# Performance work log

Hardware: AMD Instinct MI355X
Metric: run time of the kernel (lower is better)

## Reference

```python
import jax, jax.numpy as jnp
import numpy as np

B, T, D, H, L = 16, 4096, 256, 256, 2


def setup_inputs() -> dict:
    key = jax.random.key(0)
    ks = jax.random.split(key, 9)
    s = 1.0 / np.sqrt(H)
    u = lambda k, shape: jax.random.uniform(k, shape, jnp.float32, -s, s)
    return {
        "x": jax.random.normal(ks[0], (B, T, D), jnp.float32),
        "W_ih": u(ks[1], (4 * H, D)),
        "W_hh": u(ks[2], (4 * H, H)),
        "b_ih": u(ks[3], (4 * H,)),
        "b_hh": u(ks[4], (4 * H,)),
        "W_lin": u(ks[5], (L, H)),
        "b_lin": u(ks[6], (L,)),
        "fw_att": jnp.full((1, H), 0.001, jnp.float32),
        "bw_att": jnp.full((1, H), 0.001, jnp.float32),
    }


def _lstm(x, W_ih, W_hh, b_ih, b_hh):
    # x: [B, T, D] -> lstm_out: [B, T, H], torch gate order (i, f, g, o)
    x_proj = jnp.einsum("btd,gd->btg", x, W_ih) + b_ih + b_hh  # [B, T, 4H]
    h0 = jnp.zeros((x.shape[0], W_hh.shape[1]), x.dtype)
    c0 = jnp.zeros_like(h0)

    def step(carry, xp):
        h, c = carry
        gates = xp + h @ W_hh.T
        i, f, g, o = jnp.split(gates, 4, axis=-1)
        c = jax.nn.sigmoid(f) * c + jax.nn.sigmoid(i) * jnp.tanh(g)
        h = jax.nn.sigmoid(o) * jnp.tanh(c)
        return (h, c), h

    _, hs = jax.lax.scan(step, (h0, c0), jnp.swapaxes(x_proj, 0, 1))
    return jnp.swapaxes(hs, 0, 1)


def reference(x, W_ih, W_hh, b_ih, b_hh, W_lin, b_lin, fw_att, bw_att):
    lstm_out = _lstm(x, W_ih, W_hh, b_ih, b_hh)  # [B, T, H]
    logits = jnp.einsum("bth,lh->btl", lstm_out, W_lin) + b_lin
    # argmax gate is integer-valued in torch -> no grad path
    g = jax.lax.stop_gradient(jnp.argmax(logits, axis=-1).astype(lstm_out.dtype))[..., None]
    w = g * lstm_out  # [B, T, H]
    inc = jnp.cumsum(w, axis=1)
    prefix = inc - w                         # sum over j < i (exclusive)
    suffix = inc[:, -1:, :] - inc            # sum over j > i (exclusive)
    return 2.0 * lstm_out + prefix * fw_att + suffix * bw_att
```

## Files before the change

kernel.cpp:

```cpp
#include <hip/hip_runtime.h>
#include <cstdint>
#include <cstddef>

#define T_SEQ 4096
#define BATCH 16
#define HID   256
#define GATES 1024
#define DIN   256

typedef _Float16 h2 __attribute__((ext_vector_type(2)));
typedef _Float16 h8 __attribute__((ext_vector_type(8)));
typedef float    f4 __attribute__((ext_vector_type(4)));

#define NREG 100
#define LDSW_DW 28
#define LDSW_BYTES (GATES * LDSW_DW * 4)
#define HBUF_BYTES (2 * HID * 2)
#define GBUF_BYTES (2 * 2 * HID * 4)
#define K2_LDS (LDSW_BYTES + HBUF_BYTES + GBUF_BYTES + 32)

__device__ __forceinline__ float dot2f(h2 a, h2 b, float c) {
#if __has_builtin(__builtin_amdgcn_fdot2)
  return __builtin_amdgcn_fdot2(a, b, c, false);
#else
  return c + (float)a[0] * (float)b[0] + (float)a[1] * (float)b[1];
#endif
}

__device__ __forceinline__ float sigmf_(float x) {
  x = fminf(fmaxf(x, -30.0f), 30.0f);
  return 1.0f / (1.0f + __expf(-x));
}
__device__ __forceinline__ float tanhf_(float x) {
  x = fminf(fmaxf(x, -15.0f), 15.0f);
  const float e = __expf(2.0f * x);
  return (e - 1.0f) / (e + 1.0f);
}

__global__ __launch_bounds__(256) void k1_xproj(
    const float* __restrict__ x, const float* __restrict__ Wih,
    const float* __restrict__ bih, const float* __restrict__ bhh,
    _Float16* __restrict__ xp) {
  const int bid = blockIdx.x;
  const int mt = bid >> 4;
  const int nt = bid & 15;
  const int tid = threadIdx.x;
  const int wv = tid >> 6;
  const int l  = tid & 63;
  const int lr = l & 15;
  const int lq = l >> 4;

  const int arow = mt * 64 + wv * 16 + lr;
  const float* xr = x + (size_t)arow * DIN;

  f4 acc[4] = {};
  #pragma unroll
  for (int ks = 0; ks < 8; ++ks) {
    const int k0 = ks * 32 + lq * 8;
    const float4 a1 = *(const float4*)(xr + k0);
    const float4 a2 = *(const float4*)(xr + k0 + 4);
    const h8 af = { (_Float16)a1.x, (_Float16)a1.y, (_Float16)a1.z, (_Float16)a1.w,
                    (_Float16)a2.x, (_Float16)a2.y, (_Float16)a2.z, (_Float16)a2.w };
    #pragma unroll
    for (int n = 0; n < 4; ++n) {
      const int col = nt * 64 + n * 16 + lr;
      const float* wr = Wih + (size_t)col * DIN + k0;
      const float4 b1 = *(const float4*)wr;
      const float4 b2 = *(const float4*)(wr + 4);
      const h8 bf = { (_Float16)b1.x, (_Float16)b1.y, (_Float16)b1.z, (_Float16)b1.w,
                      (_Float16)b2.x, (_Float16)b2.y, (_Float16)b2.z, (_Float16)b2.w };
      acc[n] = __builtin_amdgcn_mfma_f32_16x16x32_f16(af, bf, acc[n], 0, 0, 0);
    }
  }
  #pragma unroll
  for (int n = 0; n < 4; ++n) {
    const int col = nt * 64 + n * 16 + lr;
    const float bias = bih[col] + bhh[col];
    #pragma unroll
    for (int r = 0; r < 4; ++r) {
      const int row = mt * 64 + wv * 16 + lq * 4 + r;
      xp[(size_t)row * GATES + col] = (_Float16)(acc[n][r] + bias);
    }
  }
}

__global__ __launch_bounds__(512, 2) void k2_lstm(
    const _Float16* __restrict__ xp, const float* __restrict__ Whh,
    const float* __restrict__ Wlin, const float* __restrict__ blin,
    const float* __restrict__ fw, const float* __restrict__ bw,
    float* __restrict__ out, float* __restrict__ tot) {
  extern __shared__ __align__(16) char smem[];
  h2*       ldsW  = (h2*)smem;
  _Float16* hbufP = (_Float16*)(smem + LDSW_BYTES);
  float*    gbufP = (float*)(smem + LDSW_BYTES + HBUF_BYTES);
  float*    pbufP = (float*)(smem + LDSW_BYTES + HBUF_BYTES + GBUF_BYTES);

  const int b   = blockIdx.x;
  const int tid = threadIdx.x;
  const int r0  = tid;
  const int r1  = tid + 512;
  const bool lower = (tid < 256);
  const int j = tid & 255;

  if (tid < 256) { hbufP[tid] = (_Float16)0.0f; hbufP[256 + tid] = (_Float16)0.0f; }

  h2 wA[NREG], wB[NREG];
  {
    const float2* w0p = (const float2*)(Whh + (size_t)r0 * HID);
    const float2* w1p = (const float2*)(Whh + (size_t)r1 * HID);
    #pragma unroll
    for (int i = 0; i < NREG; ++i) {
      const float2 f0 = w0p[i]; const float2 f1 = w1p[i];
      wA[i] = (h2){ (_Float16)f0.x, (_Float16)f0.y };
      wB[i] = (h2){ (_Float16)f1.x, (_Float16)f1.y };
    }
  }
  {
    const float2* wr0 = (const float2*)(Whh + (size_t)r0 * HID + 2 * NREG);
    const float2* wr1 = (const float2*)(Whh + (size_t)r1 * HID + 2 * NREG);
    #pragma unroll
    for (int i = 0; i < LDSW_DW; ++i) {
      const float2 f0 = wr0[i]; const float2 f1 = wr1[i];
      ldsW[(size_t)r0 * LDSW_DW + i] = (h2){ (_Float16)f0.x, (_Float16)f0.y };
      ldsW[(size_t)r1 * LDSW_DW + i] = (h2){ (_Float16)f1.x, (_Float16)f1.y };
    }
  }

  float fwj = 0.f, dfw = 0.f, dwj = 0.f, db = 0.f;
  if (lower) {
    fwj = fw[j];
    const float bwj = bw[j];
    dfw = fwj - bwj;
    dwj = Wlin[HID + j] - Wlin[j];
    db  = blin[1] - blin[0];
  }

  float creg = 0.0f, incj = 0.0f;

  const _Float16* xpb = xp + (size_t)b * T_SEQ * GATES;
  float* outb = out + (size_t)b * T_SEQ * HID;

  _Float16 x0a = xpb[r0],          x0b = xpb[r1];
  _Float16 x1a = xpb[GATES + r0],  x1b = xpb[GATES + r1];

  __syncthreads();

  for (int t = 0; t < T_SEQ; ++t) {
    const int pt = t & 1;
    const int pr = pt ^ 1;

    int tp = t + 2; if (tp > T_SEQ - 1) tp = T_SEQ - 1;
    const _Float16 x2a = xpb[(size_t)tp * GATES + r0];
    const _Float16 x2b = xpb[(size_t)tp * GATES + r1];

    float a0 = (float)x0a;
    float a1 = (float)x0b;

    const h8* hb8 = (const h8*)(hbufP + pr * HID);
    #pragma unroll
    for (int c = 0; c < 25; ++c) {
      const h8 hv = hb8[c];
      const h2 hp0 = { hv[0], hv[1] }, hp1 = { hv[2], hv[3] },
               hp2 = { hv[4], hv[5] }, hp3 = { hv[6], hv[7] };
      a0 = dot2f(wA[4*c+0], hp0, a0);
      a0 = dot2f(wA[4*c+1], hp1, a0);
      a0 = dot2f(wA[4*c+2], hp2, a0);
      a0 = dot2f(wA[4*c+3], hp3, a0);
      a1 = dot2f(wB[4*c+0], hp0, a1);
      a1 = dot2f(wB[4*c+1], hp1, a1);
      a1 = dot2f(wB[4*c+2], hp2, a1);
      a1 = dot2f(wB[4*c+3], hp3, a1);
    }
    const h8* w8 = (const h8*)ldsW;
    #pragma unroll
    for (int c = 0; c < 7; ++c) {
      const h8 hv = hb8[25 + c];
      const h8 u0 = w8[(size_t)r0 * 7 + c];
      const h8 u1 = w8[(size_t)r1 * 7 + c];
      const h2 hp0 = { hv[0], hv[1] }, hp1 = { hv[2], hv[3] },
               hp2 = { hv[4], hv[5] }, hp3 = { hv[6], hv[7] };
      a0 = dot2f((h2){u0[0], u0[1]}, hp0, a0);
      a0 = dot2f((h2){u0[2], u0[3]}, hp1, a0);
      a0 = dot2f((h2){u0[4], u0[5]}, hp2, a0);
      a0 = dot2f((h2){u0[6], u0[7]}, hp3, a0);
      a1 = dot2f((h2){u1[0], u1[1]}, hp0, a1);
      a1 = dot2f((h2){u1[2], u1[3]}, hp1, a1);
      a1 = dot2f((h2){u1[4], u1[5]}, hp2, a1);
      a1 = dot2f((h2){u1[6], u1[7]}, hp3, a1);
    }

    if (!lower) {
      gbufP[pt * 512 + j]       = a0;
      gbufP[pt * 512 + 256 + j] = a1;
    }
    __syncthreads();

    float hval = 0.0f;
    if (lower) {
      const float ig = sigmf_(a0);
      const float gg = tanhf_(a1);
      const float fg = sigmf_(gbufP[pt * 512 + j]);
      const float og = sigmf_(gbufP[pt * 512 + 256 + j]);
      creg = fg * creg + ig * gg;
      hval = og * tanhf_(creg);
      hbufP[pt * HID + j] = (_Float16)hval;
      float p = hval * dwj;
      #pragma unroll
      for (int off = 32; off >= 1; off >>= 1) p += __shfl_xor(p, off);
      if ((tid & 63) == 0) pbufP[pt * 4 + (tid >> 6)] = p;
    }
    __syncthreads();

    if (lower) {
      const float d = pbufP[pt*4+0] + pbufP[pt*4+1] + pbufP[pt*4+2] + pbufP[pt*4+3] + db;
      const float gf = (d > 0.0f) ? 1.0f : 0.0f;
      const float wvv = gf * hval;
      incj += wvv;
      outb[(size_t)t * HID + j] = 2.0f * hval - wvv * fwj + incj * dfw;
    }

    x0a = x1a; x0b = x1b; x1a = x2a; x1b = x2b;
  }

  if (lower) tot[b * HID + j] = incj;
}

__global__ __launch_bounds__(256) void k3_add(
    float* __restrict__ out, const float* __restrict__ tot,
    const float* __restrict__ bw) {
  const int gid = blockIdx.x * 256 + threadIdx.x;
  const size_t e = (size_t)gid * 4;
  const int b  = (int)(e >> 20);
  const int jb = ((int)(e & 255)) >> 2;
  float4 v = ((float4*)out)[gid];
  const float4 tt = ((const float4*)tot)[b * 64 + jb];
  const float4 bb = ((const float4*)bw)[jb];
  v.x += tt.x * bb.x; v.y += tt.y * bb.y;
  v.z += tt.z * bb.z; v.w += tt.w * bb.w;
  ((float4*)out)[gid] = v;
}

extern "C" void kernel_launch(void* const* d_in, const int* in_sizes, int n_in,
                              void* d_out, int out_size, void* d_ws, size_t ws_size,
                              hipStream_t stream) {
  const float* x    = (const float*)d_in[0];
  const float* Wih  = (const float*)d_in[1];
  const float* Whh  = (const float*)d_in[2];
  const float* bih  = (const float*)d_in[3];
  const float* bhh  = (const float*)d_in[4];
  const float* Wlin = (const float*)d_in[5];
  const float* blin = (const float*)d_in[6];
  const float* fw   = (const float*)d_in[7];
  const float* bw   = (const float*)d_in[8];
  float* out = (float*)d_out;

  _Float16* xp = (_Float16*)d_ws;
  float* tot = (float*)((char*)d_ws + (size_t)BATCH * T_SEQ * GATES * 2);

  k1_xproj<<<dim3(16384), dim3(256), 0, stream>>>(x, Wih, bih, bhh, xp);

  (void)hipFuncSetAttribute((const void*)k2_lstm,
                            hipFuncAttributeMaxDynamicSharedMemorySize, K2_LDS);
  k2_lstm<<<dim3(BATCH), dim3(512), K2_LDS, stream>>>(xp, Whh, Wlin, blin, fw, bw, out, tot);

  k3_add<<<dim3(16384), dim3(256), 0, stream>>>(out, tot, bw);
}
```

Baseline: 8.115 ms.

## Split LSTM recurrence across four k-quarter threads per unit pair with DPP reductions

The recurrent kernel is reorganised so each group of four threads shares two hidden units, each thread covering a quarter of the hidden dimension for all eight gate rows. Partial dot products are combined with DPP lane adds, which removes the cross-half gate buffer and one of the two per-step block barriers. Weights are split across registers, LDS and a prepacked global fp16 copy produced by a new pack kernel and reread every step. Separately, the input-projection GEMM now computes a 4x4 MFMA tile per wave so each weight load is reused across four row blocks. The cost is an extra kernel launch, per-step global weight loads, and higher register pressure.

```diff
diff --git a/kernel.cpp b/kernel.cpp
--- a/kernel.cpp
+++ b/kernel.cpp
@@ -12,12 +12,10 @@
 typedef _Float16 h8 __attribute__((ext_vector_type(8)));
 typedef float    f4 __attribute__((ext_vector_type(4)));
 
-#define NREG 100
-#define LDSW_DW 28
-#define LDSW_BYTES (GATES * LDSW_DW * 4)
-#define HBUF_BYTES (2 * HID * 2)
-#define GBUF_BYTES (2 * 2 * HID * 4)
-#define K2_LDS (LDSW_BYTES + HBUF_BYTES + GBUF_BYTES + 32)
+#define LDSW6_BYTES (512 * 128)
+#define K2HBUF      (2 * HID * 2)
+#define K2PBUF      (2 * 8 * 4)
+#define K2_LDS      (LDSW6_BYTES + K2HBUF + K2PBUF)
 
 __device__ __forceinline__ float dot2f(h2 a, h2 b, float c) {
 #if __has_builtin(__builtin_amdgcn_fdot2)
@@ -27,6 +25,20 @@
 #endif
 }
 
+template <int I>
+__device__ __forceinline__ h2 get2(h8 v) { return (h2){v[2 * I], v[2 * I + 1]}; }
+
+template <int CTRL>
+__device__ __forceinline__ float dppadd(float x) {
+  int v = __builtin_amdgcn_mov_dpp(__float_as_int(x), CTRL, 0xF, 0xF, true);
+  return x + __int_as_float(v);
+}
+
+__device__ __forceinline__ float xhalf(unsigned u, int hi) {
+  h2 p; __builtin_memcpy(&p, &u, 4);
+  return hi ? (float)p[1] : (float)p[0];
+}
+
 __device__ __forceinline__ float sigmf_(float x) {
   x = fminf(fmaxf(x, -30.0f), 30.0f);
   return 1.0f / (1.0f + __expf(-x));
@@ -35,6 +47,26 @@
   x = fminf(fmaxf(x, -15.0f), 15.0f);
   const float e = __expf(2.0f * x);
   return (e - 1.0f) / (e + 1.0f);
+}
+
+__device__ __forceinline__ h8 cvt8(float4 a, float4 b) {
+  return (h8){(_Float16)a.x, (_Float16)a.y, (_Float16)a.z, (_Float16)a.w,
+              (_Float16)b.x, (_Float16)b.y, (_Float16)b.z, (_Float16)b.w};
+}
+
+__global__ __launch_bounds__(512) void k0_pack(const float* __restrict__ Whh,
+                                               _Float16* __restrict__ wres) {
+  const int tid = threadIdx.x;
+  const int kq = tid & 3, u2 = tid >> 2;
+  const int j0 = 2 * u2, kk = kq * 64;
+  #pragma unroll
+  for (int r = 0; r < 8; ++r) {
+    const int row = (r & 3) * 256 + j0 + (r >> 2);
+    const float* wp = Whh + (size_t)row * HID + kk + 56;
+    const float4 f0 = *(const float4*)wp;
+    const float4 f1 = *(const float4*)(wp + 4);
+    *(h8*)(wres + ((size_t)r * 512 + tid) * 8) = cvt8(f0, f1);
+  }
 }
 
 __global__ __launch_bounds__(256) void k1_xproj(
@@ -42,7 +74,7 @@
     const float* __restrict__ bih, const float* __restrict__ bhh,
     _Float16* __restrict__ xp) {
   const int bid = blockIdx.x;
-  const int mt = bid >> 4;
+  const int ms = bid >> 4;
   const int nt = bid & 15;
   const int tid = threadIdx.x;
   const int wv = tid >> 6;
@@ -50,26 +82,24 @@
   const int lr = l & 15;
   const int lq = l >> 4;
 
-  const int arow = mt * 64 + wv * 16 + lr;
-  const float* xr = x + (size_t)arow * DIN;
-
-  f4 acc[4] = {};
-  #pragma unroll
+  f4 acc[4][4] = {};
   for (int ks = 0; ks < 8; ++ks) {
     const int k0 = ks * 32 + lq * 8;
-    const float4 a1 = *(const float4*)(xr + k0);
-    const float4 a2 = *(const float4*)(xr + k0 + 4);
-    const h8 af = { (_Float16)a1.x, (_Float16)a1.y, (_Float16)a1.z, (_Float16)a1.w,
-                    (_Float16)a2.x, (_Float16)a2.y, (_Float16)a2.z, (_Float16)a2.w };
+    h8 bf[4];
     #pragma unroll
     for (int n = 0; n < 4; ++n) {
       const int col = nt * 64 + n * 16 + lr;
       const float* wr = Wih + (size_t)col * DIN + k0;
-      const float4 b1 = *(const float4*)wr;
-      const float4 b2 = *(const float4*)(wr + 4);
-      const h8 bf = { (_Float16)b1.x, (_Float16)b1.y, (_Float16)b1.z, (_Float16)b1.w,
-                      (_Float16)b2.x, (_Float16)b2.y, (_Float16)b2.z, (_Float16)b2.w };
-      acc[n] = __builtin_amdgcn_mfma_f32_16x16x32_f16(af, bf, acc[n], 0, 0, 0);
+      bf[n] = cvt8(*(const float4*)wr, *(const float4*)(wr + 4));
+    }
+    #pragma unroll
+    for (int m = 0; m < 4; ++m) {
+      const int arow = ms * 256 + m * 64 + wv * 16 + lr;
+      const float* xr = x + (size_t)arow * DIN + k0;
+      const h8 af = cvt8(*(const float4*)xr, *(const float4*)(xr + 4));
+      #pragma unroll
+      for (int n = 0; n < 4; ++n)
+        acc[m][n] = __builtin_amdgcn_mfma_f32_16x16x32_f16(af, bf[n], acc[m][n], 0, 0, 0);
     }
   }
   #pragma unroll
@@ -77,152 +107,177 @@
     const int col = nt * 64 + n * 16 + lr;
     const float bias = bih[col] + bhh[col];
     #pragma unroll
-    for (int r = 0; r < 4; ++r) {
-      const int row = mt * 64 + wv * 16 + lq * 4 + r;
-      xp[(size_t)row * GATES + col] = (_Float16)(acc[n][r] + bias);
+    for (int m = 0; m < 4; ++m) {
+      #pragma unroll
+      for (int rI = 0; rI < 4; ++rI) {
+        const int row = ms * 256 + m * 64 + wv * 16 + lq * 4 + rI;
+        xp[(size_t)row * GATES + col] = (_Float16)(acc[m][n][rI] + bias);
+      }
     }
   }
 }
 
 __global__ __launch_bounds__(512, 2) void k2_lstm(
     const _Float16* __restrict__ xp, const float* __restrict__ Whh,
+    const _Float16* __restrict__ wres,
     const float* __restrict__ Wlin, const float* __restrict__ blin,
     const float* __restrict__ fw, const float* __restrict__ bw,
     float* __restrict__ out, float* __restrict__ tot) {
   extern __shared__ __align__(16) char smem[];
-  h2*       ldsW  = (h2*)smem;
-  _Float16* hbufP = (_Float16*)(smem + LDSW_BYTES);
-  float*    gbufP = (float*)(smem + LDSW_BYTES + HBUF_BYTES);
-  float*    pbufP = (float*)(smem + LDSW_BYTES + HBUF_BYTES + GBUF_BYTES);
-
-  const int b   = blockIdx.x;
-  const int tid = threadIdx.x;
-  const int r0  = tid;
-  const int r1  = tid + 512;
-  const bool lower = (tid < 256);
-  const int j = tid & 255;
-
-  if (tid < 256) { hbufP[tid] = (_Float16)0.0f; hbufP[256 + tid] = (_Float16)0.0f; }
-
-  h2 wA[NREG], wB[NREG];
-  {
-    const float2* w0p = (const float2*)(Whh + (size_t)r0 * HID);
-    const float2* w1p = (const float2*)(Whh + (size_t)r1 * HID);
-    #pragma unroll
-    for (int i = 0; i < NREG; ++i) {
-      const float2 f0 = w0p[i]; const float2 f1 = w1p[i];
-      wA[i] = (h2){ (_Float16)f0.x, (_Float16)f0.y };
-      wB[i] = (h2){ (_Float16)f1.x, (_Float16)f1.y };
-    }
-  }
-  {
-    const float2* wr0 = (const float2*)(Whh + (size_t)r0 * HID + 2 * NREG);
-    const float2* wr1 = (const float2*)(Whh + (size_t)r1 * HID + 2 * NREG);
-    #pragma unroll
-    for (int i = 0; i < LDSW_DW; ++i) {
-      const float2 f0 = wr0[i]; const float2 f1 = wr1[i];
-      ldsW[(size_t)r0 * LDSW_DW + i] = (h2){ (_Float16)f0.x, (_Float16)f0.y };
-      ldsW[(size_t)r1 * LDSW_DW + i] = (h2){ (_Float16)f1.x, (_Float16)f1.y };
-    }
-  }
-
-  float fwj = 0.f, dfw = 0.f, dwj = 0.f, db = 0.f;
-  if (lower) {
-    fwj = fw[j];
-    const float bwj = bw[j];
-    dfw = fwj - bwj;
-    dwj = Wlin[HID + j] - Wlin[j];
-    db  = blin[1] - blin[0];
-  }
-
-  float creg = 0.0f, incj = 0.0f;
-
-  const _Float16* xpb = xp + (size_t)b * T_SEQ * GATES;
+  _Float16* w6   = (_Float16*)smem;
+  _Float16* hbuf = (_Float16*)(smem + LDSW6_BYTES);
+  float*    pbuf = (float*)(smem + LDSW6_BYTES + K2HBUF);
+
+  const int b    = blockIdx.x;
+  const int tid  = threadIdx.x;
+  const int lane = tid & 63;
+  const int kq   = tid & 3;
+  const int u2   = tid >> 2;
+  const int j0   = 2 * u2;
+  const int kk   = kq * 64;
+
+  if (tid < 128) ((float*)hbuf)[tid] = 0.0f;
+
+  h8 wreg[8][6];
+  #pragma unroll
+  for (int r = 0; r < 8; ++r) {
+    const int row = (r & 3) * 256 + j0 + (r >> 2);
+    const float* wp = Whh + (size_t)row * HID + kk;
+    #pragma unroll
+    for (int c = 0; c < 6; ++c)
+      wreg[r][c] = cvt8(*(const float4*)(wp + c * 8), *(const float4*)(wp + c * 8 + 4));
+    *(h8*)(w6 + ((size_t)r * 512 + tid) * 8) =
+        cvt8(*(const float4*)(wp + 48), *(const float4*)(wp + 52));
+  }
+
+  const float fw0 = fw[j0], fw1 = fw[j0 + 1];
+  const float dfw0 = fw0 - bw[j0], dfw1 = fw1 - bw[j0 + 1];
+  const float dw0 = Wlin[HID + j0] - Wlin[j0];
+  const float dw1 = Wlin[HID + j0 + 1] - Wlin[j0 + 1];
+  const float db  = blin[1] - blin[0];
+
+  float c0 = 0.f, c1 = 0.f, inc0 = 0.f, inc1 = 0.f;
+
+  const unsigned* xpu = (const unsigned*)(xp + (size_t)b * T_SEQ * GATES);
+  const int xoff = kq * 128 + u2;
   float* outb = out + (size_t)b * T_SEQ * HID;
-
-  _Float16 x0a = xpb[r0],          x0b = xpb[r1];
-  _Float16 x1a = xpb[GATES + r0],  x1b = xpb[GATES + r1];
+  const h8* wres8 = (const h8*)wres;
+
+  unsigned xq0 = xpu[xoff];
+  unsigned xq1 = xpu[512 + xoff];
 
   __syncthreads();
 
+  #pragma unroll 1
   for (int t = 0; t < T_SEQ; ++t) {
-    const int pt = t & 1;
-    const int pr = pt ^ 1;
+    const int rb = t & 1, wb = rb ^ 1;
 
     int tp = t + 2; if (tp > T_SEQ - 1) tp = T_SEQ - 1;
-    const _Float16 x2a = xpb[(size_t)tp * GATES + r0];
-    const _Float16 x2b = xpb[(size_t)tp * GATES + r1];
-
-    float a0 = (float)x0a;
-    float a1 = (float)x0b;
-
-    const h8* hb8 = (const h8*)(hbufP + pr * HID);
-    #pragma unroll
-    for (int c = 0; c < 25; ++c) {
-      const h8 hv = hb8[c];
-      const h2 hp0 = { hv[0], hv[1] }, hp1 = { hv[2], hv[3] },
-               hp2 = { hv[4], hv[5] }, hp3 = { hv[6], hv[7] };
-      a0 = dot2f(wA[4*c+0], hp0, a0);
-      a0 = dot2f(wA[4*c+1], hp1, a0);
-      a0 = dot2f(wA[4*c+2], hp2, a0);
-      a0 = dot2f(wA[4*c+3], hp3, a0);
-      a1 = dot2f(wB[4*c+0], hp0, a1);
-      a1 = dot2f(wB[4*c+1], hp1, a1);
-      a1 = dot2f(wB[4*c+2], hp2, a1);
-      a1 = dot2f(wB[4*c+3], hp3, a1);
-    }
-    const h8* w8 = (const h8*)ldsW;
-    #pragma unroll
-    for (int c = 0; c < 7; ++c) {
-      const h8 hv = hb8[25 + c];
-      const h8 u0 = w8[(size_t)r0 * 7 + c];
-      const h8 u1 = w8[(size_t)r1 * 7 + c];
-      const h2 hp0 = { hv[0], hv[1] }, hp1 = { hv[2], hv[3] },
-               hp2 = { hv[4], hv[5] }, hp3 = { hv[6], hv[7] };
-      a0 = dot2f((h2){u0[0], u0[1]}, hp0, a0);
-      a0 = dot2f((h2){u0[2], u0[3]}, hp1, a0);
-      a0 = dot2f((h2){u0[4], u0[5]}, hp2, a0);
-      a0 = dot2f((h2){u0[6], u0[7]}, hp3, a0);
-      a1 = dot2f((h2){u1[0], u1[1]}, hp0, a1);
-      a1 = dot2f((h2){u1[2], u1[3]}, hp1, a1);
-      a1 = dot2f((h2){u1[4], u1[5]}, hp2, a1);
-      a1 = dot2f((h2){u1[6], u1[7]}, hp3, a1);
-    }
-
-    if (!lower) {
-      gbufP[pt * 512 + j]       = a0;
-      gbufP[pt * 512 + 256 + j] = a1;
-    }
+    const unsigned xq2 = xpu[(size_t)tp * 512 + xoff];
+
+    h8 w7[8];
+    #pragma unroll
+    for (int r = 0; r < 8; ++r) w7[r] = wres8[r * 512 + tid];
+
+    float acc[8] = {0.f, 0.f, 0.f, 0.f, 0.f, 0.f, 0.f, 0.f};
+    const _Float16* hb = hbuf + rb * HID + kk;
+
+    #pragma unroll
+    for (int c = 0; c < 6; ++c) {
+      const h8 hv = *(const h8*)(hb + c * 8);
+      #pragma unroll
+      for (int r = 0; r < 8; ++r) {
+        acc[r] = dot2f(get2<0>(wreg[r][c]), get2<0>(hv), acc[r]);
+        acc[r] = dot2f(get2<1>(wreg[r][c]), get2<1>(hv), acc[r]);
+        acc[r] = dot2f(get2<2>(wreg[r][c]), get2<2>(hv), acc[r]);
+        acc[r] = dot2f(get2<3>(wreg[r][c]), get2<3>(hv), acc[r]);
+      }
+    }
+    {
+      const h8 hv = *(const h8*)(hb + 48);
+      #pragma unroll
+      for (int r = 0; r < 8; ++r) {
+        const h8 wv = *(const h8*)(w6 + ((size_t)r * 512 + tid) * 8);
+        acc[r] = dot2f(get2<0>(wv), get2<0>(hv), acc[r]);
+        acc[r] = dot2f(get2<1>(wv), get2<1>(hv), acc[r]);
+        acc[r] = dot2f(get2<2>(wv), get2<2>(hv), acc[r]);
+        acc[r] = dot2f(get2<3>(wv), get2<3>(hv), acc[r]);
+      }
+    }
+    {
+      const h8 hv = *(const h8*)(hb + 56);
+      #pragma unroll
+      for (int r = 0; r < 8; ++r) {
+        acc[r] = dot2f(get2<0>(w7[r]), get2<0>(hv), acc[r]);
+        acc[r] = dot2f(get2<1>(w7[r]), get2<1>(hv), acc[r]);
+        acc[r] = dot2f(get2<2>(w7[r]), get2<2>(hv), acc[r]);
+        acc[r] = dot2f(get2<3>(w7[r]), get2<3>(hv), acc[r]);
+      }
+    }
+
+    const int xi = (int)xq0;
+    const unsigned xg0 = (unsigned)__builtin_amdgcn_mov_dpp(xi, 0x00, 0xF, 0xF, true);
+    const unsigned xg1 = (unsigned)__builtin_amdgcn_mov_dpp(xi, 0x55, 0xF, 0xF, true);
+    const unsigned xg2 = (unsigned)__builtin_amdgcn_mov_dpp(xi, 0xAA, 0xF, 0xF, true);
+    const unsigned xg3 = (unsigned)__builtin_amdgcn_mov_dpp(xi, 0xFF, 0xF, 0xF, true);
+
+    float pre[8];
+    #pragma unroll
+    for (int r = 0; r < 8; ++r) {
+      float s = acc[r];
+      s = dppadd<0xB1>(s);
+      s = dppadd<0x4E>(s);
+      pre[r] = s;
+    }
+    pre[0] += xhalf(xg0, 0); pre[4] += xhalf(xg0, 1);
+    pre[1] += xhalf(xg1, 0); pre[5] += xhalf(xg1, 1);
+    pre[2] += xhalf(xg2, 0); pre[6] += xhalf(xg2, 1);
+    pre[3] += xhalf(xg3, 0); pre[7] += xhalf(xg3, 1);
+
+    c0 = sigmf_(pre[1]) * c0 + sigmf_(pre[0]) * tanhf_(pre[2]);
+    const float h0 = sigmf_(pre[3]) * tanhf_(c0);
+    c1 = sigmf_(pre[5]) * c1 + sigmf_(pre[4]) * tanhf_(pre[6]);
+    const float h1 = sigmf_(pre[7]) * tanhf_(c1);
+
+    if (kq == 0) {
+      h2 hh = {(_Float16)h0, (_Float16)h1};
+      *(h2*)(hbuf + wb * HID + j0) = hh;
+    }
+
+    float p = (kq == 0) ? (h0 * dw0 + h1 * dw1) : 0.0f;
+    p = dppadd<0xB1>(p);
+    p = dppadd<0x4E>(p);
+    p = dppadd<0x124>(p);
+    p = dppadd<0x128>(p);
+    p = dppadd<0x142>(p);
+    p = dppadd<0x143>(p);
+    if (lane == 63) pbuf[rb * 8 + (tid >> 6)] = p;
+
     __syncthreads();
 
-    float hval = 0.0f;
-    if (lower) {
-      const float ig = sigmf_(a0);
-      const float gg = tanhf_(a1);
-      const float fg = sigmf_(gbufP[pt * 512 + j]);
-      const float og = sigmf_(gbufP[pt * 512 + 256 + j]);
-      creg = fg * creg + ig * gg;
-      hval = og * tanhf_(creg);
-      hbufP[pt * HID + j] = (_Float16)hval;
-      float p = hval * dwj;
-      #pragma unroll
-      for (int off = 32; off >= 1; off >>= 1) p += __shfl_xor(p, off);
-      if ((tid & 63) == 0) pbufP[pt * 4 + (tid >> 6)] = p;
-    }
-    __syncthreads();
-
-    if (lower) {
-      const float d = pbufP[pt*4+0] + pbufP[pt*4+1] + pbufP[pt*4+2] + pbufP[pt*4+3] + db;
-      const float gf = (d > 0.0f) ? 1.0f : 0.0f;
-      const float wvv = gf * hval;
-      incj += wvv;
-      outb[(size_t)t * HID + j] = 2.0f * hval - wvv * fwj + incj * dfw;
-    }
-
-    x0a = x1a; x0b = x1b; x1a = x2a; x1b = x2b;
-  }
-
-  if (lower) tot[b * HID + j] = incj;
+    float pv = pbuf[rb * 8 + (lane & 7)];
+    pv = dppadd<0xB1>(pv);
+    pv = dppadd<0x4E>(pv);
+    pv = dppadd<0x12C>(pv);
+    const float d = pv + db;
+    const float gf = (d > 0.0f) ? 1.0f : 0.0f;
+
+    if (kq == 0) {
+      const float wv0 = gf * h0, wv1 = gf * h1;
+      inc0 += wv0; inc1 += wv1;
+      float2 ov;
+      ov.x = 2.0f * h0 - wv0 * fw0 + inc0 * dfw0;
+      ov.y = 2.0f * h1 - wv1 * fw1 + inc1 * dfw1;
+      *(float2*)(outb + (size_t)t * HID + j0) = ov;
+    }
+
+    xq0 = xq1; xq1 = xq2;
+  }
+
+  if (kq == 0) {
+    float2 tv; tv.x = inc0; tv.y = inc1;
+    *(float2*)(tot + b * HID + j0) = tv;
+  }
 }
 
 __global__ __launch_bounds__(256) void k3_add(
@@ -254,14 +309,18 @@
   const float* bw   = (const float*)d_in[8];
   float* out = (float*)d_out;
 
-  _Float16* xp = (_Float16*)d_ws;
-  float* tot = (float*)((char*)d_ws + (size_t)BATCH * T_SEQ * GATES * 2);
-
-  k1_xproj<<<dim3(16384), dim3(256), 0, stream>>>(x, Wih, bih, bhh, xp);
+  _Float16* xpw  = (_Float16*)d_ws;
+  float*    tot  = (float*)((char*)d_ws + (size_t)BATCH * T_SEQ * GATES * 2);
+  _Float16* wres = (_Float16*)((char*)d_ws + (size_t)BATCH * T_SEQ * GATES * 2 + 16384);
+
+  k0_pack<<<dim3(1), dim3(512), 0, stream>>>(Whh, wres);
+
+  k1_xproj<<<dim3(4096), dim3(256), 0, stream>>>(x, Wih, bih, bhh, xpw);
 
   (void)hipFuncSetAttribute((const void*)k2_lstm,
                             hipFuncAttributeMaxDynamicSharedMemorySize, K2_LDS);
-  k2_lstm<<<dim3(BATCH), dim3(512), K2_LDS, stream>>>(xp, Whh, Wlin, blin, fw, bw, out, tot);
+  k2_lstm<<<dim3(BATCH), dim3(512), K2_LDS, stream>>>(xpw, Whh, wres, Wlin, blin,
+                                                      fw, bw, out, tot);
 
   k3_add<<<dim3(16384), dim3(256), 0, stream>>>(out, tot, bw);
 }
```

Measured after the change: 12.95 ms. 59.6% more time.
